# Kernel optimization log

Measured on AMD Instinct MI355X. Metric: run time of the kernel, lower is better.

The kernel has to match this reference:

```python
import jax, jax.numpy as jnp
import numpy as np

N = 100000      # nodes
E = 1600000     # edges (before self loops)
IN_DIM, EMB, HID, OUT, L = 128, 128, 128, 64, 3
LN_EPS = 1e-5


def _lin(k, fi, fo):
    return (jax.random.normal(k, (fi, fo), jnp.float32) / np.sqrt(fi)).astype(jnp.float32)


def setup_inputs() -> dict:
    key = jax.random.key(0)
    ks = jax.random.split(key, 8)
    x = jax.random.normal(ks[0], (N, IN_DIM), jnp.float32)
    edge_index = jax.random.randint(ks[1], (2, E), 0, N, dtype=jnp.int64)
    # in-degree of destination nodes (as data.degree would provide)
    degree = jnp.zeros((N,), jnp.float32).at[edge_index[1]].add(1.0)
    lks = jax.random.split(ks[2], 2 * L)
    W1 = jnp.stack([_lin(lks[2 * i], EMB, HID) for i in range(L)])
    W2 = jnp.stack([_lin(lks[2 * i + 1], HID, EMB) for i in range(L)])
    return dict(
        x=x, edge_index=edge_index, degree=degree,
        Win=_lin(ks[3], IN_DIM, EMB), b_in=jnp.zeros((EMB,), jnp.float32),
        W1=W1, b1=jnp.zeros((L, HID), jnp.float32),
        W2=W2, b2=jnp.zeros((L, EMB), jnp.float32),
        ln_g=jnp.ones((L, EMB), jnp.float32), ln_b=jnp.zeros((L, EMB), jnp.float32),
        out_g=jnp.ones((EMB,), jnp.float32), out_b=jnp.zeros((EMB,), jnp.float32),
        Wout=_lin(ks[4], EMB, OUT), b_out=jnp.zeros((OUT,), jnp.float32),
    )


def _layernorm(h, g, b):
    m = h.mean(-1, keepdims=True)
    v = ((h - m) ** 2).mean(-1, keepdims=True)
    return (h - m) * jax.lax.rsqrt(v + LN_EPS) * g + b


def reference(x, edge_index, degree, Win, b_in, W1, b1, W2, b2,
              ln_g, ln_b, out_g, out_b, Wout, b_out):
    # input_lin: Linear -> Dropout(eval: identity) -> ReLU
    h = jax.nn.relu(x @ Win + b_in)                        # [N, EMB]
    # add self loops, degree + 1
    loop = jnp.arange(N, dtype=edge_index.dtype)
    src = jnp.concatenate([edge_index[0], loop])           # [E+N]
    dst = jnp.concatenate([edge_index[1], loop])
    inv = jax.lax.rsqrt(degree + 1.0)                      # deg^{-1/2}
    coef = (inv[src] * inv[dst])[:, None]                  # symmetric GCN norm
    for i in range(L):
        m = h @ W1[i] + b1[i]                              # [N, HID]
        agg = jax.ops.segment_sum(m[src] * coef, dst, num_segments=N)  # gather-scatter
        out = agg @ W2[i] + b2[i]                          # [N, EMB]
        h = jax.nn.relu(_layernorm(out + h, ln_g[i], ln_b[i]))  # residual + LN + act (dropout=id)
    h = _layernorm(h, out_g, out_b)
    return h @ Wout + b_out
```

## Files before the change

kernel.cpp:

```cpp
#include <hip/hip_runtime.h>
#include <cstdint>
#include <cstddef>

typedef unsigned short u16;
typedef unsigned int u32;
typedef __attribute__((ext_vector_type(2))) unsigned short u16x2;
typedef __attribute__((ext_vector_type(4))) unsigned short u16x4;
typedef __attribute__((ext_vector_type(8))) unsigned short u16x8;
typedef __attribute__((ext_vector_type(8))) __bf16 bf16x8;
typedef __attribute__((ext_vector_type(4))) float f32x4;

#define PREP_F32  0
#define PREP_BF16 1
#define PREP_LN   2
#define EPI_IN    0
#define EPI_SCALE 1
#define EPI_LNRES 2
#define EPI_NONE  3

__device__ __forceinline__ float wred(float v) {
#pragma unroll
  for (int m = 32; m >= 1; m >>= 1) v += __shfl_xor(v, m, 64);
  return v;
}
__device__ __forceinline__ u16 f2bf(float f) {
  u32 u = __float_as_uint(f);
  u += 0x7fffu + ((u >> 16) & 1u);
  return (u16)(u >> 16);
}
__device__ __forceinline__ float bflo(u32 u) { return __uint_as_float(u << 16); }
__device__ __forceinline__ float bfhi(u32 u) { return __uint_as_float(u & 0xffff0000u); }
__device__ __forceinline__ u32 pack2(float a, float b) {
  u32 ua = __float_as_uint(a); ua += 0x7fffu + ((ua >> 16) & 1u);
  u32 ub = __float_as_uint(b); ub += 0x7fffu + ((ub >> 16) & 1u);
  return (ua >> 16) | (ub & 0xffff0000u);
}

__global__ void scan_block_k(const float* __restrict__ deg, int* __restrict__ offs,
                             int* __restrict__ bsum, int N) {
  __shared__ int sh[256];
  int tid = threadIdx.x;
  int i = blockIdx.x * 256 + tid;
  int c = (i < N) ? (int)(deg[i] + 0.5f) : 0;
  int val = c;
  for (int off = 1; off < 256; off <<= 1) {
    sh[tid] = val; __syncthreads();
    if (tid >= off) val += sh[tid - off];
    __syncthreads();
  }
  if (i < N) offs[i] = val - c;
  if (tid == 255) bsum[blockIdx.x] = val;
}

__global__ void scan_bsum_k(int* __restrict__ bsum, int nb) {
  __shared__ int sh[1024];
  int tid = threadIdx.x;
  int c = (tid < nb) ? bsum[tid] : 0;
  int val = c;
  for (int off = 1; off < 1024; off <<= 1) {
    sh[tid] = val; __syncthreads();
    if (tid >= off) val += sh[tid - off];
    __syncthreads();
  }
  if (tid < nb) bsum[tid] = val - c;
}

__global__ void scan_add_k(int* __restrict__ offs, const int* __restrict__ bsum,
                           int* __restrict__ gcur, float* __restrict__ inv,
                           const float* __restrict__ deg, int N, int E) {
  int i = blockIdx.x * 256 + threadIdx.x;
  if (i < N) {
    int o = offs[i] + bsum[i >> 8];
    offs[i] = o;
    inv[i] = rsqrtf(deg[i] + 1.0f);
    if ((i & 511) == 0) gcur[i >> 9] = o;
  } else if (i == N) {
    offs[N] = E;
  }
}

__global__ __launch_bounds__(256) void scatter_k(
    const int* __restrict__ src, const int* __restrict__ dst,
    int* __restrict__ gcur, uint2* __restrict__ pairs, int E) {
  __shared__ int hist[256];
  __shared__ int base_[256];
  const int tid = threadIdx.x;
  const int e0 = blockIdx.x * 8192;
  const int e1 = min(E, e0 + 8192);
  hist[tid] = 0;
  __syncthreads();
  for (int e = e0 + tid; e < e1; e += 256)
    atomicAdd(&hist[dst[e] >> 9], 1);
  __syncthreads();
  int c = hist[tid];
  if (c > 0) base_[tid] = atomicAdd(&gcur[tid], c);
  hist[tid] = 0;
  __syncthreads();
  for (int e = e0 + tid; e < e1; e += 256) {
    int d = dst[e];
    int b = d >> 9;
    int r = atomicAdd(&hist[b], 1);
    pairs[base_[b] + r] = make_uint2((u32)src[e], (u32)d);
  }
}

__global__ __launch_bounds__(256) void fill2_k(
    const uint2* __restrict__ pairs, const int* __restrict__ offs,
    int* __restrict__ col, int N) {
  __shared__ int cur[512];
  const int b = blockIdx.x;
  const int n0 = b << 9;
  const int n1 = min(N, n0 + 512);
  const int tid = threadIdx.x;
  for (int i = tid; i < n1 - n0; i += 256) cur[i] = offs[n0 + i];
  __syncthreads();
  const int e0 = offs[n0], e1 = offs[n1];
  for (int e = e0 + tid; e < e1; e += 256) {
    uint2 pr = pairs[e];
    int p = atomicAdd(&cur[(int)pr.y - n0], 1);
    col[p] = (int)pr.x;
  }
}

__global__ __launch_bounds__(256) void spmm_k(
    const uint4* __restrict__ msc, const int* __restrict__ offs,
    const int* __restrict__ col, const float* __restrict__ inv,
    uint4* __restrict__ agg, int N) {
  const int wid = threadIdx.x >> 6, lane = threadIdx.x & 63;
  const int d = blockIdx.x * 4 + wid;
  if (d >= N) return;
  const int g = lane >> 4, c = lane & 15;
  const int s0 = offs[d], s1 = offs[d + 1];
  float2 a0 = {0.f, 0.f}, a1 = {0.f, 0.f}, a2 = {0.f, 0.f}, a3 = {0.f, 0.f};
  int base = s0;
  const int nfull = s0 + ((s1 - s0) & ~15);
  for (; base < nfull; base += 16) {
    int sA = col[base + g];
    int sB = col[base + 4 + g];
    int sC = col[base + 8 + g];
    int sD = col[base + 12 + g];
    uint4 rA = msc[(size_t)sA * 16 + c];
    uint4 rB = msc[(size_t)sB * 16 + c];
    uint4 rC = msc[(size_t)sC * 16 + c];
    uint4 rD = msc[(size_t)sD * 16 + c];
    a0.x += bflo(rA.x); a0.y += bfhi(rA.x);
    a1.x += bflo(rA.y); a1.y += bfhi(rA.y);
    a2.x += bflo(rA.z); a2.y += bfhi(rA.z);
    a3.x += bflo(rA.w); a3.y += bfhi(rA.w);
    a0.x += bflo(rB.x); a0.y += bfhi(rB.x);
    a1.x += bflo(rB.y); a1.y += bfhi(rB.y);
    a2.x += bflo(rB.z); a2.y += bfhi(rB.z);
    a3.x += bflo(rB.w); a3.y += bfhi(rB.w);
    a0.x += bflo(rC.x); a0.y += bfhi(rC.x);
    a1.x += bflo(rC.y); a1.y += bfhi(rC.y);
    a2.x += bflo(rC.z); a2.y += bfhi(rC.z);
    a3.x += bflo(rC.w); a3.y += bfhi(rC.w);
    a0.x += bflo(rD.x); a0.y += bfhi(rD.x);
    a1.x += bflo(rD.y); a1.y += bfhi(rD.y);
    a2.x += bflo(rD.z); a2.y += bfhi(rD.z);
    a3.x += bflo(rD.w); a3.y += bfhi(rD.w);
  }
  if (base < s1) {
    const int last = s1 - 1;
    int jj0 = base + g;
    int jj1 = base + 4 + g;
    int jj2 = base + 8 + g;
    int jj3 = base + 12 + g;
    int sA = col[min(jj0, last)];
    int sB = col[min(jj1, last)];
    int sC = col[min(jj2, last)];
    int sD = col[min(jj3, last)];
    uint4 rA = msc[(size_t)sA * 16 + c];
    uint4 rB = msc[(size_t)sB * 16 + c];
    uint4 rC = msc[(size_t)sC * 16 + c];
    uint4 rD = msc[(size_t)sD * 16 + c];
    float mA = (jj0 <= last) ? 1.f : 0.f;
    float mB = (jj1 <= last) ? 1.f : 0.f;
    float mC = (jj2 <= last) ? 1.f : 0.f;
    float mD = (jj3 <= last) ? 1.f : 0.f;
    a0.x = fmaf(mA, bflo(rA.x), a0.x); a0.y = fmaf(mA, bfhi(rA.x), a0.y);
    a1.x = fmaf(mA, bflo(rA.y), a1.x); a1.y = fmaf(mA, bfhi(rA.y), a1.y);
    a2.x = fmaf(mA, bflo(rA.z), a2.x); a2.y = fmaf(mA, bfhi(rA.z), a2.y);
    a3.x = fmaf(mA, bflo(rA.w), a3.x); a3.y = fmaf(mA, bfhi(rA.w), a3.y);
    a0.x = fmaf(mB, bflo(rB.x), a0.x); a0.y = fmaf(mB, bfhi(rB.x), a0.y);
    a1.x = fmaf(mB, bflo(rB.y), a1.x); a1.y = fmaf(mB, bfhi(rB.y), a1.y);
    a2.x = fmaf(mB, bflo(rB.z), a2.x); a2.y = fmaf(mB, bfhi(rB.z), a2.y);
    a3.x = fmaf(mB, bflo(rB.w), a3.x); a3.y = fmaf(mB, bfhi(rB.w), a3.y);
    a0.x = fmaf(mC, bflo(rC.x), a0.x); a0.y = fmaf(mC, bfhi(rC.x), a0.y);
    a1.x = fmaf(mC, bflo(rC.y), a1.x); a1.y = fmaf(mC, bfhi(rC.y), a1.y);
    a2.x = fmaf(mC, bflo(rC.z), a2.x); a2.y = fmaf(mC, bfhi(rC.z), a2.y);
    a3.x = fmaf(mC, bflo(rC.w), a3.x); a3.y = fmaf(mC, bfhi(rC.w), a3.y);
    a0.x = fmaf(mD, bflo(rD.x), a0.x); a0.y = fmaf(mD, bfhi(rD.x), a0.y);
    a1.x = fmaf(mD, bflo(rD.y), a1.x); a1.y = fmaf(mD, bfhi(rD.y), a1.y);
    a2.x = fmaf(mD, bflo(rD.z), a2.x); a2.y = fmaf(mD, bfhi(rD.z), a2.y);
    a3.x = fmaf(mD, bflo(rD.w), a3.x); a3.y = fmaf(mD, bfhi(rD.w), a3.y);
  }
  a0.x += __shfl_xor(a0.x, 16, 64); a0.x += __shfl_xor(a0.x, 32, 64);
  a0.y += __shfl_xor(a0.y, 16, 64); a0.y += __shfl_xor(a0.y, 32, 64);
  a1.x += __shfl_xor(a1.x, 16, 64); a1.x += __shfl_xor(a1.x, 32, 64);
  a1.y += __shfl_xor(a1.y, 16, 64); a1.y += __shfl_xor(a1.y, 32, 64);
  a2.x += __shfl_xor(a2.x, 16, 64); a2.x += __shfl_xor(a2.x, 32, 64);
  a2.y += __shfl_xor(a2.y, 16, 64); a2.y += __shfl_xor(a2.y, 32, 64);
  a3.x += __shfl_xor(a3.x, 16, 64); a3.x += __shfl_xor(a3.x, 32, 64);
  a3.y += __shfl_xor(a3.y, 16, 64); a3.y += __shfl_xor(a3.y, 32, 64);
  if (g == 0) {
    uint4 r = msc[(size_t)d * 16 + c];
    float iv = inv[d];
    uint4 o;
    o.x = pack2((a0.x + bflo(r.x)) * iv, (a0.y + bfhi(r.x)) * iv);
    o.y = pack2((a1.x + bflo(r.y)) * iv, (a1.y + bfhi(r.y)) * iv);
    o.z = pack2((a2.x + bflo(r.z)) * iv, (a2.y + bfhi(r.z)) * iv);
    o.w = pack2((a3.x + bflo(r.w)) * iv, (a3.y + bfhi(r.w)) * iv);
    agg[(size_t)d * 16 + c] = o;
  }
}

__global__ void pack_w_k(const float* __restrict__ W, u16* __restrict__ P, int ncol) {
  int t = blockIdx.x * 256 + threadIdx.x;
  int NT = ncol >> 4;
  int total = 4 * NT * 64;
  if (t >= total) return;
  int lane = t & 63;
  int tmp = t >> 6;
  int nt = tmp % NT, kc = tmp / NT;
  int n = nt * 16 + (lane & 15);
  int kb = kc * 32 + ((lane >> 4) << 2);
  u16* dst = P + (size_t)t * 8;
#pragma unroll
  for (int j = 0; j < 8; ++j) {
    int k = kb + (j & 3) + ((j >> 2) << 4);
    dst[j] = f2bf(W[(size_t)k * ncol + n]);
  }
}

template <int NOUT, int PREP, int EPI>
__global__ __launch_bounds__(256) void gemm_mfma(
    const void* __restrict__ Xv, const u16* __restrict__ Wp,
    const float* __restrict__ bias, void* __restrict__ Yv,
    const void* __restrict__ resv,
    const float* __restrict__ g1, const float* __restrict__ lb1,
    int N) {
  constexpr int NT = NOUT / 16;
  __shared__ union {
    u16  xs[32][136];
    float cs[32][132];
  } sh;
  const int tid = threadIdx.x;
  const int lane = tid & 63, wid = tid >> 6;
  const int row0 = blockIdx.x * 32;

  if constexpr (PREP == PREP_F32) {
    const float* X = (const float*)Xv;
    for (int i = tid; i < 1024; i += 256) {
      int r = i >> 5, c4 = i & 31;
      float4 v = ((const float4*)(X + (size_t)(row0 + r) * 128))[c4];
      u16x4 o = {f2bf(v.x), f2bf(v.y), f2bf(v.z), f2bf(v.w)};
      *(u16x4*)&sh.xs[r][c4 * 4] = o;
    }
  } else if constexpr (PREP == PREP_BF16) {
    const u16x4* X = (const u16x4*)Xv;
    for (int i = tid; i < 1024; i += 256) {
      int r = i >> 5, c4 = i & 31;
      *(u16x4*)&sh.xs[r][c4 * 4] = X[(size_t)(row0 + r) * 32 + c4];
    }
  } else {
    const u32* X = (const u32*)Xv;
    float2 gg = *(const float2*)&g1[lane * 2];
    float2 bb = *(const float2*)&lb1[lane * 2];
    for (int rr = 0; rr < 8; ++rr) {
      int r = wid * 8 + rr;
      u32 v = X[(size_t)(row0 + r) * 64 + lane];
      float tx = bflo(v), ty = bfhi(v);
      float mean = wred(tx + ty) * (1.f / 128.f);
      float dx = tx - mean, dy = ty - mean;
      float var = wred(dx * dx + dy * dy) * (1.f / 128.f);
      float rstd = rsqrtf(var + 1e-5f);
      u16x2 o = {f2bf(dx * rstd * gg.x + bb.x), f2bf(dy * rstd * gg.y + bb.y)};
      *(u16x2*)&sh.xs[r][lane * 2] = o;
    }
  }
  __syncthreads();

  constexpr int NTW = (NOUT == 128) ? 4 : 2;
  const int m0  = (NOUT == 128) ? ((wid >> 1) << 4) : ((wid & 1) << 4);
  const int ntb = (NOUT == 128) ? ((wid & 1) << 2) : ((wid >> 1) << 1);

  f32x4 acc[NTW];
#pragma unroll
  for (int t = 0; t < NTW; ++t) acc[t] = (f32x4){0.f, 0.f, 0.f, 0.f};

  const int ar  = m0 + (lane & 15);
  const int akb = (lane >> 4) << 2;
  const bf16x8* Bp = (const bf16x8*)Wp;
#pragma unroll
  for (int kc = 0; kc < 4; ++kc) {
    u16x4 lo = *(const u16x4*)&sh.xs[ar][kc * 32 + akb];
    u16x4 hi = *(const u16x4*)&sh.xs[ar][kc * 32 + akb + 16];
    u16x8 av;
#pragma unroll
    for (int j = 0; j < 4; ++j) { av[j] = lo[j]; av[j + 4] = hi[j]; }
    bf16x8 a = __builtin_bit_cast(bf16x8, av);
#pragma unroll
    for (int t = 0; t < NTW; ++t) {
      bf16x8 b = Bp[(kc * NT + ntb + t) * 64 + lane];
      acc[t] = __builtin_amdgcn_mfma_f32_16x16x32_bf16(a, b, acc[t], 0, 0, 0);
    }
  }

  const int cb = lane & 15;
  const int rg = (lane >> 4) << 2;
  if constexpr (EPI == EPI_NONE) {
    float* Y = (float*)Yv;
#pragma unroll
    for (int t = 0; t < NTW; ++t) {
      int col = (ntb + t) * 16 + cb;
      float bv = bias[col];
#pragma unroll
      for (int r = 0; r < 4; ++r) {
        int gr = row0 + m0 + rg + r;
        Y[(size_t)gr * NOUT + col] = acc[t][r] + bv;
      }
    }
  } else if constexpr (EPI == EPI_SCALE) {
    const float* inv = (const float*)resv;
    u16* Y = (u16*)Yv;
#pragma unroll
    for (int t = 0; t < NTW; ++t) {
      int col = (ntb + t) * 16 + cb;
      float bv = bias[col];
#pragma unroll
      for (int r = 0; r < 4; ++r) {
        int gr = row0 + m0 + rg + r;
        Y[(size_t)gr * NOUT + col] = f2bf((acc[t][r] + bv) * inv[gr]);
      }
    }
  } else {
    __syncthreads();
#pragma unroll
    for (int t = 0; t < NTW; ++t) {
      int col = (ntb + t) * 16 + cb;
      float bv = bias[col];
#pragma unroll
      for (int r = 0; r < 4; ++r) sh.cs[m0 + rg + r][col] = acc[t][r] + bv;
    }
    __syncthreads();
    u32* Y = (u32*)Yv;
    if constexpr (EPI == EPI_IN) {
      for (int rr = 0; rr < 8; ++rr) {
        int r = wid * 8 + rr;
        int gr = row0 + r;
        float2 t2 = *(const float2*)&sh.cs[r][lane * 2];
        Y[(size_t)gr * 64 + lane] = pack2(fmaxf(t2.x, 0.f), fmaxf(t2.y, 0.f));
      }
    } else {
      const u32* res = (const u32*)resv;
      float2 gg = *(const float2*)&g1[lane * 2];
      float2 bb = *(const float2*)&lb1[lane * 2];
      for (int rr = 0; rr < 8; ++rr) {
        int r = wid * 8 + rr;
        int gr = row0 + r;
        float2 t2 = *(const float2*)&sh.cs[r][lane * 2];
        u32 hv = res[(size_t)gr * 64 + lane];
        float tx = t2.x + bflo(hv), ty = t2.y + bfhi(hv);
        float mean = wred(tx + ty) * (1.f / 128.f);
        float dx = tx - mean, dy = ty - mean;
        float var = wred(dx * dx + dy * dy) * (1.f / 128.f);
        float rstd = rsqrtf(var + 1e-5f);
        float y0 = fmaxf(dx * rstd * gg.x + bb.x, 0.f);
        float y1 = fmaxf(dy * rstd * gg.y + bb.y, 0.f);
        Y[(size_t)gr * 64 + lane] = pack2(y0, y1);
      }
    }
  }
}

extern "C" void kernel_launch(void* const* d_in, const int* in_sizes, int n_in,
                              void* d_out, int out_size, void* d_ws, size_t ws_size,
                              hipStream_t stream) {
  (void)n_in; (void)out_size; (void)ws_size;
  const float* x      = (const float*)d_in[0];
  const int*   eidx   = (const int*)d_in[1];
  const float* degree = (const float*)d_in[2];
  const float* Win    = (const float*)d_in[3];
  const float* b_in   = (const float*)d_in[4];
  const float* W1     = (const float*)d_in[5];
  const float* b1     = (const float*)d_in[6];
  const float* W2     = (const float*)d_in[7];
  const float* b2     = (const float*)d_in[8];
  const float* ln_g   = (const float*)d_in[9];
  const float* ln_b   = (const float*)d_in[10];
  const float* out_g  = (const float*)d_in[11];
  const float* out_b  = (const float*)d_in[12];
  const float* Wout   = (const float*)d_in[13];
  const float* b_out  = (const float*)d_in[14];

  const int N = in_sizes[0] / 128;
  const int E = in_sizes[1] / 2;
  const int* esrc = eidx;
  const int* edst = eidx + E;

  char* p = (char*)d_ws;
  auto alloc = [&](size_t bytes) {
    char* q = p;
    p += (bytes + 255) & ~(size_t)255;
    return q;
  };
  float* inv    = (float*)alloc((size_t)N * 4);
  int*   offs   = (int*)alloc(((size_t)N + 1) * 4);
  int*   gcur   = (int*)alloc(256 * 4);
  int*   bsum   = (int*)alloc(1024 * 4);
  int*   col    = (int*)alloc((size_t)E * 4);
  uint2* pairs  = (uint2*)alloc((size_t)E * 8);
  u32*   h      = (u32*)alloc((size_t)N * 128 * 2);
  u32*   msc    = (u32*)alloc((size_t)N * 128 * 2);
  u32*   agg    = (u32*)alloc((size_t)N * 128 * 2);
  u16*   pWin   = (u16*)alloc(4 * 8 * 64 * 8 * 2);
  u16*   pWout  = (u16*)alloc(4 * 4 * 64 * 8 * 2);
  u16*   pW1    = (u16*)alloc(3 * 4 * 8 * 64 * 8 * 2);
  u16*   pW2    = (u16*)alloc(3 * 4 * 8 * 64 * 8 * 2);

  pack_w_k<<<8, 256, 0, stream>>>(Win, pWin, 128);
  for (int l = 0; l < 3; ++l) {
    pack_w_k<<<8, 256, 0, stream>>>(W1 + (size_t)l * 128 * 128, pW1 + (size_t)l * 16384, 128);
    pack_w_k<<<8, 256, 0, stream>>>(W2 + (size_t)l * 128 * 128, pW2 + (size_t)l * 16384, 128);
  }
  pack_w_k<<<4, 256, 0, stream>>>(Wout, pWout, 64);

  const int nb = (N + 255) / 256;
  const int NB = (N + 511) / 512;
  scan_block_k<<<nb, 256, 0, stream>>>(degree, offs, bsum, N);
  scan_bsum_k<<<1, 1024, 0, stream>>>(bsum, nb);
  scan_add_k<<<(N + 256) / 256, 256, 0, stream>>>(offs, bsum, gcur, inv, degree, N, E);
  scatter_k<<<(E + 8191) / 8192, 256, 0, stream>>>(esrc, edst, gcur, pairs, E);
  fill2_k<<<NB, 256, 0, stream>>>(pairs, offs, col, N);

  const int gemmGrid = (N + 31) / 32;
  const int rowGrid  = (N + 3) / 4;

  gemm_mfma<128, PREP_F32, EPI_IN><<<gemmGrid, 256, 0, stream>>>(
      x, pWin, b_in, h, nullptr, nullptr, nullptr, N);
  for (int l = 0; l < 3; ++l) {
    gemm_mfma<128, PREP_BF16, EPI_SCALE><<<gemmGrid, 256, 0, stream>>>(
        h, pW1 + (size_t)l * 16384, b1 + l * 128, msc, inv, nullptr, nullptr, N);
    spmm_k<<<rowGrid, 256, 0, stream>>>((const uint4*)msc, offs, col, inv, (uint4*)agg, N);
    gemm_mfma<128, PREP_BF16, EPI_LNRES><<<gemmGrid, 256, 0, stream>>>(
        agg, pW2 + (size_t)l * 16384, b2 + l * 128, h, h,
        ln_g + l * 128, ln_b + l * 128, N);
  }
  gemm_mfma<64, PREP_LN, EPI_NONE><<<gemmGrid, 256, 0, stream>>>(
      h, pWout, b_out, d_out, nullptr, out_g, out_b, N);
}
```

Before: 411.8 us.

## Fuse SpMM aggregation with W2 GEMM and LayerNorm epilogue; merge weight packing

After: 391.3 us. -5.0%, faster.

```diff
diff --git a/kernel.cpp b/kernel.cpp
--- a/kernel.cpp
+++ b/kernel.cpp
@@ -10,12 +10,11 @@
 typedef __attribute__((ext_vector_type(8))) __bf16 bf16x8;
 typedef __attribute__((ext_vector_type(4))) float f32x4;
 
-#define PREP_F32  0
-#define PREP_BF16 1
-#define PREP_LN   2
+#define PREP_F32   0
+#define PREP_BF16  1
+#define PREP_LN    2
 #define EPI_IN    0
 #define EPI_SCALE 1
-#define EPI_LNRES 2
 #define EPI_NONE  3
 
 __device__ __forceinline__ float wred(float v) {
@@ -122,101 +121,16 @@
   }
 }
 
-__global__ __launch_bounds__(256) void spmm_k(
-    const uint4* __restrict__ msc, const int* __restrict__ offs,
-    const int* __restrict__ col, const float* __restrict__ inv,
-    uint4* __restrict__ agg, int N) {
-  const int wid = threadIdx.x >> 6, lane = threadIdx.x & 63;
-  const int d = blockIdx.x * 4 + wid;
-  if (d >= N) return;
-  const int g = lane >> 4, c = lane & 15;
-  const int s0 = offs[d], s1 = offs[d + 1];
-  float2 a0 = {0.f, 0.f}, a1 = {0.f, 0.f}, a2 = {0.f, 0.f}, a3 = {0.f, 0.f};
-  int base = s0;
-  const int nfull = s0 + ((s1 - s0) & ~15);
-  for (; base < nfull; base += 16) {
-    int sA = col[base + g];
-    int sB = col[base + 4 + g];
-    int sC = col[base + 8 + g];
-    int sD = col[base + 12 + g];
-    uint4 rA = msc[(size_t)sA * 16 + c];
-    uint4 rB = msc[(size_t)sB * 16 + c];
-    uint4 rC = msc[(size_t)sC * 16 + c];
-    uint4 rD = msc[(size_t)sD * 16 + c];
-    a0.x += bflo(rA.x); a0.y += bfhi(rA.x);
-    a1.x += bflo(rA.y); a1.y += bfhi(rA.y);
-    a2.x += bflo(rA.z); a2.y += bfhi(rA.z);
-    a3.x += bflo(rA.w); a3.y += bfhi(rA.w);
-    a0.x += bflo(rB.x); a0.y += bfhi(rB.x);
-    a1.x += bflo(rB.y); a1.y += bfhi(rB.y);
-    a2.x += bflo(rB.z); a2.y += bfhi(rB.z);
-    a3.x += bflo(rB.w); a3.y += bfhi(rB.w);
-    a0.x += bflo(rC.x); a0.y += bfhi(rC.x);
-    a1.x += bflo(rC.y); a1.y += bfhi(rC.y);
-    a2.x += bflo(rC.z); a2.y += bfhi(rC.z);
-    a3.x += bflo(rC.w); a3.y += bfhi(rC.w);
-    a0.x += bflo(rD.x); a0.y += bfhi(rD.x);
-    a1.x += bflo(rD.y); a1.y += bfhi(rD.y);
-    a2.x += bflo(rD.z); a2.y += bfhi(rD.z);
-    a3.x += bflo(rD.w); a3.y += bfhi(rD.w);
-  }
-  if (base < s1) {
-    const int last = s1 - 1;
-    int jj0 = base + g;
-    int jj1 = base + 4 + g;
-    int jj2 = base + 8 + g;
-    int jj3 = base + 12 + g;
-    int sA = col[min(jj0, last)];
-    int sB = col[min(jj1, last)];
-    int sC = col[min(jj2, last)];
-    int sD = col[min(jj3, last)];
-    uint4 rA = msc[(size_t)sA * 16 + c];
-    uint4 rB = msc[(size_t)sB * 16 + c];
-    uint4 rC = msc[(size_t)sC * 16 + c];
-    uint4 rD = msc[(size_t)sD * 16 + c];
-    float mA = (jj0 <= last) ? 1.f : 0.f;
-    float mB = (jj1 <= last) ? 1.f : 0.f;
-    float mC = (jj2 <= last) ? 1.f : 0.f;
-    float mD = (jj3 <= last) ? 1.f : 0.f;
-    a0.x = fmaf(mA, bflo(rA.x), a0.x); a0.y = fmaf(mA, bfhi(rA.x), a0.y);
-    a1.x = fmaf(mA, bflo(rA.y), a1.x); a1.y = fmaf(mA, bfhi(rA.y), a1.y);
-    a2.x = fmaf(mA, bflo(rA.z), a2.x); a2.y = fmaf(mA, bfhi(rA.z), a2.y);
-    a3.x = fmaf(mA, bflo(rA.w), a3.x); a3.y = fmaf(mA, bfhi(rA.w), a3.y);
-    a0.x = fmaf(mB, bflo(rB.x), a0.x); a0.y = fmaf(mB, bfhi(rB.x), a0.y);
-    a1.x = fmaf(mB, bflo(rB.y), a1.x); a1.y = fmaf(mB, bfhi(rB.y), a1.y);
-    a2.x = fmaf(mB, bflo(rB.z), a2.x); a2.y = fmaf(mB, bfhi(rB.z), a2.y);
-    a3.x = fmaf(mB, bflo(rB.w), a3.x); a3.y = fmaf(mB, bfhi(rB.w), a3.y);
-    a0.x = fmaf(mC, bflo(rC.x), a0.x); a0.y = fmaf(mC, bfhi(rC.x), a0.y);
-    a1.x = fmaf(mC, bflo(rC.y), a1.x); a1.y = fmaf(mC, bfhi(rC.y), a1.y);
-    a2.x = fmaf(mC, bflo(rC.z), a2.x); a2.y = fmaf(mC, bfhi(rC.z), a2.y);
-    a3.x = fmaf(mC, bflo(rC.w), a3.x); a3.y = fmaf(mC, bfhi(rC.w), a3.y);
-    a0.x = fmaf(mD, bflo(rD.x), a0.x); a0.y = fmaf(mD, bfhi(rD.x), a0.y);
-    a1.x = fmaf(mD, bflo(rD.y), a1.x); a1.y = fmaf(mD, bfhi(rD.y), a1.y);
-    a2.x = fmaf(mD, bflo(rD.z), a2.x); a2.y = fmaf(mD, bfhi(rD.z), a2.y);
-    a3.x = fmaf(mD, bflo(rD.w), a3.x); a3.y = fmaf(mD, bfhi(rD.w), a3.y);
-  }
-  a0.x += __shfl_xor(a0.x, 16, 64); a0.x += __shfl_xor(a0.x, 32, 64);
-  a0.y += __shfl_xor(a0.y, 16, 64); a0.y += __shfl_xor(a0.y, 32, 64);
-  a1.x += __shfl_xor(a1.x, 16, 64); a1.x += __shfl_xor(a1.x, 32, 64);
-  a1.y += __shfl_xor(a1.y, 16, 64); a1.y += __shfl_xor(a1.y, 32, 64);
-  a2.x += __shfl_xor(a2.x, 16, 64); a2.x += __shfl_xor(a2.x, 32, 64);
-  a2.y += __shfl_xor(a2.y, 16, 64); a2.y += __shfl_xor(a2.y, 32, 64);
-  a3.x += __shfl_xor(a3.x, 16, 64); a3.x += __shfl_xor(a3.x, 32, 64);
-  a3.y += __shfl_xor(a3.y, 16, 64); a3.y += __shfl_xor(a3.y, 32, 64);
-  if (g == 0) {
-    uint4 r = msc[(size_t)d * 16 + c];
-    float iv = inv[d];
-    uint4 o;
-    o.x = pack2((a0.x + bflo(r.x)) * iv, (a0.y + bfhi(r.x)) * iv);
-    o.y = pack2((a1.x + bflo(r.y)) * iv, (a1.y + bfhi(r.y)) * iv);
-    o.z = pack2((a2.x + bflo(r.z)) * iv, (a2.y + bfhi(r.z)) * iv);
-    o.w = pack2((a3.x + bflo(r.w)) * iv, (a3.y + bfhi(r.w)) * iv);
-    agg[(size_t)d * 16 + c] = o;
-  }
-}
-
-__global__ void pack_w_k(const float* __restrict__ W, u16* __restrict__ P, int ncol) {
-  int t = blockIdx.x * 256 + threadIdx.x;
+__global__ void pack_all_k(const float* __restrict__ Win, const float* __restrict__ W1,
+                           const float* __restrict__ W2, const float* __restrict__ Wout,
+                           u16* __restrict__ pWin, u16* __restrict__ pW1,
+                           u16* __restrict__ pW2, u16* __restrict__ pWout) {
+  const int b = blockIdx.x;
+  const float* W; u16* P; int ncol; int t;
+  if (b < 8)       { W = Win;                        P = pWin;                      ncol = 128; t = b * 256 + threadIdx.x; }
+  else if (b < 32) { int l = (b - 8) / 8;  W = W1 + (size_t)l * 16384;  P = pW1 + (size_t)l * 16384; ncol = 128; t = ((b - 8) % 8) * 256 + threadIdx.x; }
+  else if (b < 56) { int l = (b - 32) / 8; W = W2 + (size_t)l * 16384;  P = pW2 + (size_t)l * 16384; ncol = 128; t = ((b - 32) % 8) * 256 + threadIdx.x; }
+  else             { W = Wout;                       P = pWout;                     ncol = 64;  t = (b - 56) * 256 + threadIdx.x; }
   int NT = ncol >> 4;
   int total = 4 * NT * 64;
   if (t >= total) return;
@@ -230,6 +144,158 @@
   for (int j = 0; j < 8; ++j) {
     int k = kb + (j & 3) + ((j >> 2) << 4);
     dst[j] = f2bf(W[(size_t)k * ncol + n]);
+  }
+}
+
+__global__ __launch_bounds__(256) void spmm_gemm_k(
+    const uint4* __restrict__ msc, const int* __restrict__ offs,
+    const int* __restrict__ col, const float* __restrict__ inv,
+    const u16* __restrict__ Wp, const float* __restrict__ bias,
+    u32* __restrict__ h, const float* __restrict__ g1,
+    const float* __restrict__ lb1, int N) {
+  __shared__ union {
+    u16  xs[32][136];
+    float cs[32][132];
+  } sh;
+  const int tid = threadIdx.x;
+  const int lane = tid & 63, wid = tid >> 6;
+  const int row0 = blockIdx.x * 32;
+  const int g = lane >> 4, c = lane & 15;
+
+  for (int rr = 0; rr < 8; ++rr) {
+    const int d = row0 + wid * 8 + rr;
+    const int s0 = offs[d], s1 = offs[d + 1];
+    float2 a0 = {0.f, 0.f}, a1 = {0.f, 0.f}, a2 = {0.f, 0.f}, a3 = {0.f, 0.f};
+    int base = s0;
+    const int nfull = s0 + ((s1 - s0) & ~15);
+    for (; base < nfull; base += 16) {
+      int sA = col[base + g];
+      int sB = col[base + 4 + g];
+      int sC = col[base + 8 + g];
+      int sD = col[base + 12 + g];
+      uint4 rA = msc[(size_t)sA * 16 + c];
+      uint4 rB = msc[(size_t)sB * 16 + c];
+      uint4 rC = msc[(size_t)sC * 16 + c];
+      uint4 rD = msc[(size_t)sD * 16 + c];
+      a0.x += bflo(rA.x); a0.y += bfhi(rA.x);
+      a1.x += bflo(rA.y); a1.y += bfhi(rA.y);
+      a2.x += bflo(rA.z); a2.y += bfhi(rA.z);
+      a3.x += bflo(rA.w); a3.y += bfhi(rA.w);
+      a0.x += bflo(rB.x); a0.y += bfhi(rB.x);
+      a1.x += bflo(rB.y); a1.y += bfhi(rB.y);
+      a2.x += bflo(rB.z); a2.y += bfhi(rB.z);
+      a3.x += bflo(rB.w); a3.y += bfhi(rB.w);
+      a0.x += bflo(rC.x); a0.y += bfhi(rC.x);
+      a1.x += bflo(rC.y); a1.y += bfhi(rC.y);
+      a2.x += bflo(rC.z); a2.y += bfhi(rC.z);
+      a3.x += bflo(rC.w); a3.y += bfhi(rC.w);
+      a0.x += bflo(rD.x); a0.y += bfhi(rD.x);
+      a1.x += bflo(rD.y); a1.y += bfhi(rD.y);
+      a2.x += bflo(rD.z); a2.y += bfhi(rD.z);
+      a3.x += bflo(rD.w); a3.y += bfhi(rD.w);
+    }
+    if (base < s1) {
+      const int last = s1 - 1;
+      int jA = base + g, jB = base + 4 + g, jC = base + 8 + g, jD = base + 12 + g;
+      int sA = col[min(jA, last)];
+      int sB = col[min(jB, last)];
+      int sC = col[min(jC, last)];
+      int sD = col[min(jD, last)];
+      uint4 rA = msc[(size_t)sA * 16 + c];
+      uint4 rB = msc[(size_t)sB * 16 + c];
+      uint4 rC = msc[(size_t)sC * 16 + c];
+      uint4 rD = msc[(size_t)sD * 16 + c];
+      float mA = (jA <= last) ? 1.f : 0.f;
+      float mB = (jB <= last) ? 1.f : 0.f;
+      float mC = (jC <= last) ? 1.f : 0.f;
+      float mD = (jD <= last) ? 1.f : 0.f;
+      a0.x = fmaf(mA, bflo(rA.x), a0.x); a0.y = fmaf(mA, bfhi(rA.x), a0.y);
+      a1.x = fmaf(mA, bflo(rA.y), a1.x); a1.y = fmaf(mA, bfhi(rA.y), a1.y);
+      a2.x = fmaf(mA, bflo(rA.z), a2.x); a2.y = fmaf(mA, bfhi(rA.z), a2.y);
+      a3.x = fmaf(mA, bflo(rA.w), a3.x); a3.y = fmaf(mA, bfhi(rA.w), a3.y);
+      a0.x = fmaf(mB, bflo(rB.x), a0.x); a0.y = fmaf(mB, bfhi(rB.x), a0.y);
+      a1.x = fmaf(mB, bflo(rB.y), a1.x); a1.y = fmaf(mB, bfhi(rB.y), a1.y);
+      a2.x = fmaf(mB, bflo(rB.z), a2.x); a2.y = fmaf(mB, bfhi(rB.z), a2.y);
+      a3.x = fmaf(mB, bflo(rB.w), a3.x); a3.y = fmaf(mB, bfhi(rB.w), a3.y);
+      a0.x = fmaf(mC, bflo(rC.x), a0.x); a0.y = fmaf(mC, bfhi(rC.x), a0.y);
+      a1.x = fmaf(mC, bflo(rC.y), a1.x); a1.y = fmaf(mC, bfhi(rC.y), a1.y);
+      a2.x = fmaf(mC, bflo(rC.z), a2.x); a2.y = fmaf(mC, bfhi(rC.z), a2.y);
+      a3.x = fmaf(mC, bflo(rC.w), a3.x); a3.y = fmaf(mC, bfhi(rC.w), a3.y);
+      a0.x = fmaf(mD, bflo(rD.x), a0.x); a0.y = fmaf(mD, bfhi(rD.x), a0.y);
+      a1.x = fmaf(mD, bflo(rD.y), a1.x); a1.y = fmaf(mD, bfhi(rD.y), a1.y);
+      a2.x = fmaf(mD, bflo(rD.z), a2.x); a2.y = fmaf(mD, bfhi(rD.z), a2.y);
+      a3.x = fmaf(mD, bflo(rD.w), a3.x); a3.y = fmaf(mD, bfhi(rD.w), a3.y);
+    }
+    a0.x += __shfl_xor(a0.x, 16, 64); a0.x += __shfl_xor(a0.x, 32, 64);
+    a0.y += __shfl_xor(a0.y, 16, 64); a0.y += __shfl_xor(a0.y, 32, 64);
+    a1.x += __shfl_xor(a1.x, 16, 64); a1.x += __shfl_xor(a1.x, 32, 64);
+    a1.y += __shfl_xor(a1.y, 16, 64); a1.y += __shfl_xor(a1.y, 32, 64);
+    a2.x += __shfl_xor(a2.x, 16, 64); a2.x += __shfl_xor(a2.x, 32, 64);
+    a2.y += __shfl_xor(a2.y, 16, 64); a2.y += __shfl_xor(a2.y, 32, 64);
+    a3.x += __shfl_xor(a3.x, 16, 64); a3.x += __shfl_xor(a3.x, 32, 64);
+    a3.y += __shfl_xor(a3.y, 16, 64); a3.y += __shfl_xor(a3.y, 32, 64);
+    if (g == 0) {
+      uint4 r = msc[(size_t)d * 16 + c];
+      float iv = inv[d];
+      uint4 o;
+      o.x = pack2((a0.x + bflo(r.x)) * iv, (a0.y + bfhi(r.x)) * iv);
+      o.y = pack2((a1.x + bflo(r.y)) * iv, (a1.y + bfhi(r.y)) * iv);
+      o.z = pack2((a2.x + bflo(r.z)) * iv, (a2.y + bfhi(r.z)) * iv);
+      o.w = pack2((a3.x + bflo(r.w)) * iv, (a3.y + bfhi(r.w)) * iv);
+      *(uint4*)&sh.xs[wid * 8 + rr][c * 8] = o;
+    }
+  }
+  __syncthreads();
+
+  const int m0  = (wid >> 1) << 4;
+  const int ntb = (wid & 1) << 2;
+  f32x4 acc[4];
+#pragma unroll
+  for (int t = 0; t < 4; ++t) acc[t] = (f32x4){0.f, 0.f, 0.f, 0.f};
+  const int ar  = m0 + (lane & 15);
+  const int akb = (lane >> 4) << 2;
+  const bf16x8* Bp = (const bf16x8*)Wp;
+#pragma unroll
+  for (int kc = 0; kc < 4; ++kc) {
+    u16x4 lo = *(const u16x4*)&sh.xs[ar][kc * 32 + akb];
+    u16x4 hi = *(const u16x4*)&sh.xs[ar][kc * 32 + akb + 16];
+    u16x8 av;
+#pragma unroll
+    for (int j = 0; j < 4; ++j) { av[j] = lo[j]; av[j + 4] = hi[j]; }
+    bf16x8 a = __builtin_bit_cast(bf16x8, av);
+#pragma unroll
+    for (int t = 0; t < 4; ++t) {
+      bf16x8 b = Bp[(kc * 8 + ntb + t) * 64 + lane];
+      acc[t] = __builtin_amdgcn_mfma_f32_16x16x32_bf16(a, b, acc[t], 0, 0, 0);
+    }
+  }
+
+  const int cb = lane & 15;
+  const int rg = (lane >> 4) << 2;
+  __syncthreads();
+#pragma unroll
+  for (int t = 0; t < 4; ++t) {
+    int colm = (ntb + t) * 16 + cb;
+    float bv = bias[colm];
+#pragma unroll
+    for (int r = 0; r < 4; ++r) sh.cs[m0 + rg + r][colm] = acc[t][r] + bv;
+  }
+  __syncthreads();
+  float2 gg = *(const float2*)&g1[lane * 2];
+  float2 bb = *(const float2*)&lb1[lane * 2];
+  for (int rr = 0; rr < 8; ++rr) {
+    int r = wid * 8 + rr;
+    int gr = row0 + r;
+    float2 t2 = *(const float2*)&sh.cs[r][lane * 2];
+    u32 hv = h[(size_t)gr * 64 + lane];
+    float tx = t2.x + bflo(hv), ty = t2.y + bfhi(hv);
+    float mean = wred(tx + ty) * (1.f / 128.f);
+    float dx = tx - mean, dy = ty - mean;
+    float var = wred(dx * dx + dy * dy) * (1.f / 128.f);
+    float rstd = rsqrtf(var + 1e-5f);
+    float y0 = fmaxf(dx * rstd * gg.x + bb.x, 0.f);
+    float y1 = fmaxf(dy * rstd * gg.y + bb.y, 0.f);
+    h[(size_t)gr * 64 + lane] = pack2(y0, y1);
   }
 }
 
@@ -345,31 +411,11 @@
     }
     __syncthreads();
     u32* Y = (u32*)Yv;
-    if constexpr (EPI == EPI_IN) {
-      for (int rr = 0; rr < 8; ++rr) {
-        int r = wid * 8 + rr;
-        int gr = row0 + r;
-        float2 t2 = *(const float2*)&sh.cs[r][lane * 2];
-        Y[(size_t)gr * 64 + lane] = pack2(fmaxf(t2.x, 0.f), fmaxf(t2.y, 0.f));
-      }
-    } else {
-      const u32* res = (const u32*)resv;
-      float2 gg = *(const float2*)&g1[lane * 2];
-      float2 bb = *(const float2*)&lb1[lane * 2];
-      for (int rr = 0; rr < 8; ++rr) {
-        int r = wid * 8 + rr;
-        int gr = row0 + r;
-        float2 t2 = *(const float2*)&sh.cs[r][lane * 2];
-        u32 hv = res[(size_t)gr * 64 + lane];
-        float tx = t2.x + bflo(hv), ty = t2.y + bfhi(hv);
-        float mean = wred(tx + ty) * (1.f / 128.f);
-        float dx = tx - mean, dy = ty - mean;
-        float var = wred(dx * dx + dy * dy) * (1.f / 128.f);
-        float rstd = rsqrtf(var + 1e-5f);
-        float y0 = fmaxf(dx * rstd * gg.x + bb.x, 0.f);
-        float y1 = fmaxf(dy * rstd * gg.y + bb.y, 0.f);
-        Y[(size_t)gr * 64 + lane] = pack2(y0, y1);
-      }
+    for (int rr = 0; rr < 8; ++rr) {
+      int r = wid * 8 + rr;
+      int gr = row0 + r;
+      float2 t2 = *(const float2*)&sh.cs[r][lane * 2];
+      Y[(size_t)gr * 64 + lane] = pack2(fmaxf(t2.x, 0.f), fmaxf(t2.y, 0.f));
     }
   }
 }
@@ -413,18 +459,12 @@
   uint2* pairs  = (uint2*)alloc((size_t)E * 8);
   u32*   h      = (u32*)alloc((size_t)N * 128 * 2);
   u32*   msc    = (u32*)alloc((size_t)N * 128 * 2);
-  u32*   agg    = (u32*)alloc((size_t)N * 128 * 2);
   u16*   pWin   = (u16*)alloc(4 * 8 * 64 * 8 * 2);
   u16*   pWout  = (u16*)alloc(4 * 4 * 64 * 8 * 2);
   u16*   pW1    = (u16*)alloc(3 * 4 * 8 * 64 * 8 * 2);
   u16*   pW2    = (u16*)alloc(3 * 4 * 8 * 64 * 8 * 2);
 
-  pack_w_k<<<8, 256, 0, stream>>>(Win, pWin, 128);
-  for (int l = 0; l < 3; ++l) {
-    pack_w_k<<<8, 256, 0, stream>>>(W1 + (size_t)l * 128 * 128, pW1 + (size_t)l * 16384, 128);
-    pack_w_k<<<8, 256, 0, stream>>>(W2 + (size_t)l * 128 * 128, pW2 + (size_t)l * 16384, 128);
-  }
-  pack_w_k<<<4, 256, 0, stream>>>(Wout, pWout, 64);
+  pack_all_k<<<60, 256, 0, stream>>>(Win, W1, W2, Wout, pWin, pW1, pW2, pWout);
 
   const int nb = (N + 255) / 256;
   const int NB = (N + 511) / 512;
@@ -435,17 +475,15 @@
   fill2_k<<<NB, 256, 0, stream>>>(pairs, offs, col, N);
 
   const int gemmGrid = (N + 31) / 32;
-  const int rowGrid  = (N + 3) / 4;
 
   gemm_mfma<128, PREP_F32, EPI_IN><<<gemmGrid, 256, 0, stream>>>(
       x, pWin, b_in, h, nullptr, nullptr, nullptr, N);
   for (int l = 0; l < 3; ++l) {
     gemm_mfma<128, PREP_BF16, EPI_SCALE><<<gemmGrid, 256, 0, stream>>>(
         h, pW1 + (size_t)l * 16384, b1 + l * 128, msc, inv, nullptr, nullptr, N);
-    spmm_k<<<rowGrid, 256, 0, stream>>>((const uint4*)msc, offs, col, inv, (uint4*)agg, N);
-    gemm_mfma<128, PREP_BF16, EPI_LNRES><<<gemmGrid, 256, 0, stream>>>(
-        agg, pW2 + (size_t)l * 16384, b2 + l * 128, h, h,
-        ln_g + l * 128, ln_b + l * 128, N);
+    spmm_gemm_k<<<gemmGrid, 256, 0, stream>>>(
+        (const uint4*)msc, offs, col, inv, pW2 + (size_t)l * 16384,
+        b2 + l * 128, h, ln_g + l * 128, ln_b + l * 128, N);
   }
   gemm_mfma<64, PREP_LN, EPI_NONE><<<gemmGrid, 256, 0, stream>>>(
       h, pWout, b_out, d_out, nullptr, out_g, out_b, N);
```
